# Kernel tuning notes

Hardware: AMD Instinct MI355X
Metric: run time of the kernel (lower is better)

Reference implementation:

```python
import jax, jax.numpy as jnp
import numpy as np

N, F, P, E, HID = 50000, 4, 12, 1_600_000, 64  # nodes, input feats, periods (FH), edges, hidden


def setup_inputs() -> dict:
    key = jax.random.key(0)
    ks = jax.random.split(key, 16)

    def nrm(k, shp, scale=0.1):
        return jax.random.normal(k, shp, jnp.float32) * scale

    inp = {
        "x": jax.random.normal(ks[0], (N, F, P), jnp.float32),
        "edge_index": jax.random.randint(ks[1], (2, E), 0, N),
        "edge_weights": jax.random.uniform(ks[2], (E,), jnp.float32),
        "att": nrm(ks[3], (P,), 1.0),
    }
    i = 4
    for g in ("z", "r", "h"):  # TGCN gate params: GCNConv weight/bias + Linear(2*hid, hid)
        inp[f"Wg_{g}"] = nrm(ks[i], (F, HID))
        inp[f"bg_{g}"] = jnp.zeros((HID,), jnp.float32)
        inp[f"Wl_{g}"] = nrm(jax.random.fold_in(ks[i], 1), (2 * HID, HID))
        inp[f"bl_{g}"] = jnp.zeros((HID,), jnp.float32)
        i += 1
    for j in range(1, 5):
        inp[f"W{j}"] = nrm(ks[i], (HID, HID))
        inp[f"b{j}"] = jnp.zeros((HID,), jnp.float32)
        i += 1
    inp["Wo"] = nrm(ks[i], (HID, P * F))
    inp["bo"] = jnp.zeros((P * F,), jnp.float32)
    return inp


def _gcn_norm(edge_index, ew):
    # GCNConv default: add self loops (weight 1), symmetric D^-1/2 (A+I) D^-1/2 normalization
    src, dst = edge_index[0], edge_index[1]
    loop = jnp.arange(N)
    src_f = jnp.concatenate([src, loop])
    dst_f = jnp.concatenate([dst, loop])
    ew_f = jnp.concatenate([ew, jnp.ones((N,), ew.dtype)])
    deg = jax.ops.segment_sum(ew_f, dst_f, num_segments=N)
    dinv = jnp.where(deg > 0, jax.lax.rsqrt(deg), 0.0)
    norm = dinv[src_f] * ew_f * dinv[dst_f]
    return src_f, dst_f, norm


def _gcn(x, W, b, src, dst, norm):
    xw = x @ W                               # [N, HID] transform before propagate
    msg = xw[src] * norm[:, None]            # gather + scale, [E+N, HID]
    return jax.ops.segment_sum(msg, dst, num_segments=N) + b


def reference(x, edge_index, edge_weights, att,
              Wg_z, bg_z, Wl_z, bl_z,
              Wg_r, bg_r, Wl_r, bl_r,
              Wg_h, bg_h, Wl_h, bl_h,
              W1, b1, W2, b2, W3, b3, W4, b4, Wo, bo):
    src, dst, norm = _gcn_norm(edge_index, edge_weights)

    def tgcn_cell(xt):
        # A3TGCN passes H=None every period -> H starts at zeros each period
        Hz = jnp.zeros((xt.shape[0], HID), xt.dtype)
        z = jax.nn.sigmoid(jnp.concatenate([_gcn(xt, Wg_z, bg_z, src, dst, norm), Hz], -1) @ Wl_z + bl_z)
        r = jax.nn.sigmoid(jnp.concatenate([_gcn(xt, Wg_r, bg_r, src, dst, norm), Hz], -1) @ Wl_r + bl_r)
        htil = jnp.tanh(jnp.concatenate([_gcn(xt, Wg_h, bg_h, src, dst, norm), Hz * r], -1) @ Wl_h + bl_h)
        return z * Hz + (1.0 - z) * htil

    probs = jax.nn.softmax(att)
    h = jnp.zeros((N, HID), x.dtype)
    for p in range(P):  # small fixed period loop keeps peak memory at one period's messages
        h = h + probs[p] * tgcn_cell(x[:, :, p])

    h = jax.nn.relu(h)
    h = h @ W1 + b1
    h = h @ W2 + b2
    h = h @ W3 + b3
    h = h @ W4 + b4
    h = h @ Wo + bo                          # [N, FH*F]
    return h.reshape(-1, F, P)
```

## Files before the change

### kernel.cpp

```cpp
#include <hip/hip_runtime.h>
#include <hip/hip_fp16.h>

#define FP 48
#define HID 64
#define NP 12
#define PL 65
#define NBLK 256
#define CAPB 9216

__device__ __forceinline__ void mm_stage(const float* __restrict__ Alds,
                                         const float* __restrict__ Wg,
                                         float* __restrict__ Clds, int t)
{
    const int rg = (t >> 4) * 4, cg = (t & 15) * 4;
    float acc[4][4] = {};
    for (int k = 0; k < 64; ++k) {
        float a0 = Alds[(rg + 0) * PL + k];
        float a1 = Alds[(rg + 1) * PL + k];
        float a2 = Alds[(rg + 2) * PL + k];
        float a3 = Alds[(rg + 3) * PL + k];
        const float4 bv = *reinterpret_cast<const float4*>(Wg + k * 64 + cg);
        acc[0][0] += a0 * bv.x; acc[0][1] += a0 * bv.y; acc[0][2] += a0 * bv.z; acc[0][3] += a0 * bv.w;
        acc[1][0] += a1 * bv.x; acc[1][1] += a1 * bv.y; acc[1][2] += a1 * bv.z; acc[1][3] += a1 * bv.w;
        acc[2][0] += a2 * bv.x; acc[2][1] += a2 * bv.y; acc[2][2] += a2 * bv.z; acc[2][3] += a2 * bv.w;
        acc[3][0] += a3 * bv.x; acc[3][1] += a3 * bv.y; acc[3][2] += a3 * bv.z; acc[3][3] += a3 * bv.w;
    }
    for (int i = 0; i < 4; ++i)
        for (int j = 0; j < 4; ++j)
            Clds[(rg + i) * PL + cg + j] = acc[i][j];
}

__device__ __forceinline__ void bias_stage(const float* __restrict__ bin,
                                           const float* __restrict__ Wg,
                                           const float* __restrict__ badd,
                                           float* __restrict__ bout, int t)
{
    if (t < 64) {
        float s = badd[t];
        for (int k = 0; k < 64; ++k) s += bin[k] * Wg[k * 64 + t];
        bout[t] = s;
    }
}

__device__ void do_prep(
    const float* __restrict__ att,
    const float* __restrict__ Wg_z, const float* __restrict__ bg_z,
    const float* __restrict__ Wl_z, const float* __restrict__ bl_z,
    const float* __restrict__ Wg_h, const float* __restrict__ bg_h,
    const float* __restrict__ Wl_h, const float* __restrict__ bl_h,
    const float* __restrict__ W1, const float* __restrict__ b1,
    const float* __restrict__ W2, const float* __restrict__ b2,
    const float* __restrict__ W3, const float* __restrict__ b3,
    const float* __restrict__ W4, const float* __restrict__ b4,
    const float* __restrict__ Wo, const float* __restrict__ bo,
    float* __restrict__ probs, float* __restrict__ Mz, float* __restrict__ cz,
    float* __restrict__ Mh, float* __restrict__ ch,
    float* __restrict__ Wc, float* __restrict__ bc, int t)
{
    __shared__ float A[64 * PL];
    __shared__ float B[64 * PL];
    __shared__ float bias[64];
    __shared__ float bias2[64];

    if (t == 0) {
        float m = att[0];
        for (int p = 1; p < NP; ++p) m = fmaxf(m, att[p]);
        float e[NP]; float s = 0.f;
        for (int p = 0; p < NP; ++p) { e[p] = __expf(att[p] - m); s += e[p]; }
        float inv = 1.f / s;
        for (int p = 0; p < NP; ++p) probs[p] = e[p] * inv;
    }

    {
        int f = t >> 6, j = t & 63;
        float az = 0.f, ah = 0.f;
        for (int k = 0; k < HID; ++k) {
            az += Wg_z[f * HID + k] * Wl_z[k * HID + j];
            ah += Wg_h[f * HID + k] * Wl_h[k * HID + j];
        }
        Mz[t] = az; Mh[t] = ah;
    }
    if (t < HID) {
        float az = bl_z[t], ah = bl_h[t];
        for (int k = 0; k < HID; ++k) {
            az += bg_z[k] * Wl_z[k * HID + t];
            ah += bg_h[k] * Wl_h[k * HID + t];
        }
        cz[t] = az; ch[t] = ah;
    }

    for (int idx = t; idx < 4096; idx += 256) {
        int i = idx >> 6, j = idx & 63;
        A[i * PL + j] = W1[idx];
    }
    if (t < 64) bias[t] = b1[t];
    __syncthreads();

    mm_stage(A, W2, B, t);
    bias_stage(bias, W2, b2, bias2, t);
    __syncthreads();
    mm_stage(B, W3, A, t);
    bias_stage(bias2, W3, b3, bias, t);
    __syncthreads();
    mm_stage(A, W4, B, t);
    bias_stage(bias, W4, b4, bias2, t);
    __syncthreads();

    const int rg = (t >> 4) * 4, cg = (t & 15) * 4;
    if (cg < FP) {
        float acc[4][4] = {};
        for (int k = 0; k < 64; ++k) {
            float a0 = B[(rg + 0) * PL + k];
            float a1 = B[(rg + 1) * PL + k];
            float a2 = B[(rg + 2) * PL + k];
            float a3 = B[(rg + 3) * PL + k];
            const float4 bv = *reinterpret_cast<const float4*>(Wo + k * FP + cg);
            acc[0][0] += a0 * bv.x; acc[0][1] += a0 * bv.y; acc[0][2] += a0 * bv.z; acc[0][3] += a0 * bv.w;
            acc[1][0] += a1 * bv.x; acc[1][1] += a1 * bv.y; acc[1][2] += a1 * bv.z; acc[1][3] += a1 * bv.w;
            acc[2][0] += a2 * bv.x; acc[2][1] += a2 * bv.y; acc[2][2] += a2 * bv.z; acc[2][3] += a2 * bv.w;
            acc[3][0] += a3 * bv.x; acc[3][1] += a3 * bv.y; acc[3][2] += a3 * bv.z; acc[3][3] += a3 * bv.w;
        }
        for (int i = 0; i < 4; ++i)
            for (int j = 0; j < 4; ++j)
                Wc[(rg + i) * FP + cg + j] = acc[i][j];
    }
    if (t < FP) {
        float s = bo[t];
        for (int k = 0; k < 64; ++k) s += bias2[k] * Wo[k * FP + t];
        bc[t] = s;
    }
}

__global__ __launch_bounds__(256) void build_kernel(
    const int* __restrict__ src, const int* __restrict__ dst,
    const float* __restrict__ ew,
    unsigned* __restrict__ cursor, int2* __restrict__ binned,
    int E, int CE, int NBUK,
    const float* __restrict__ att,
    const float* __restrict__ Wg_z, const float* __restrict__ bg_z,
    const float* __restrict__ Wl_z, const float* __restrict__ bl_z,
    const float* __restrict__ Wg_h, const float* __restrict__ bg_h,
    const float* __restrict__ Wl_h, const float* __restrict__ bl_h,
    const float* __restrict__ W1, const float* __restrict__ b1,
    const float* __restrict__ W2, const float* __restrict__ b2,
    const float* __restrict__ W3, const float* __restrict__ b3,
    const float* __restrict__ W4, const float* __restrict__ b4,
    const float* __restrict__ Wo, const float* __restrict__ bo,
    float* __restrict__ probs, float* __restrict__ Mz, float* __restrict__ cz,
    float* __restrict__ Mh, float* __restrict__ ch,
    float* __restrict__ Wc, float* __restrict__ bc)
{
    const int t = threadIdx.x;
    if (blockIdx.x == NBLK) {
        do_prep(att, Wg_z, bg_z, Wl_z, bl_z, Wg_h, bg_h, Wl_h, bl_h,
                W1, b1, W2, b2, W3, b3, W4, b4, Wo, bo,
                probs, Mz, cz, Mh, ch, Wc, bc, t);
        return;
    }
    __shared__ int cnt[256];
    __shared__ int off[256];
    for (int i = t; i < NBUK; i += 256) cnt[i] = 0;
    __syncthreads();
    const int base = blockIdx.x * CE;
    const int endb = min(base + CE, E);
    for (int e = base + t; e < endb; e += 256)
        atomicAdd(&cnt[((unsigned)dst[e]) >> 8], 1);
    __syncthreads();
    for (int i = t; i < NBUK; i += 256)
        off[i] = (int)atomicAdd(&cursor[i], (unsigned)cnt[i]);
    __syncthreads();
    for (int e = base + t; e < endb; e += 256) {
        const int d = dst[e];
        const int b = ((unsigned)d) >> 8;
        const int r = atomicAdd(&off[b], 1);
        if (r < CAPB)
            binned[(size_t)b * CAPB + r] =
                make_int2(((d & 255) << 16) | src[e], __float_as_int(ew[e]));
    }
}

__global__ __launch_bounds__(256) void csr_convert_kernel(
    const int2* __restrict__ binned, const unsigned* __restrict__ cursor,
    unsigned* __restrict__ csr, int2* __restrict__ nodeinfo,
    const float* __restrict__ x,
    unsigned short* __restrict__ xs, int N, int NBUK)
{
    const int t = threadIdx.x;
    const int b = blockIdx.x;
    const int node0 = b << 8;
    const int nend = min(256, N - node0);
    const int ebeg = b * CAPB;
    const int ecnt = min((int)cursor[b], CAPB);
    const int eend = ebeg + ecnt;

    __shared__ int   cnt[256];
    __shared__ float fsum[256];
    __shared__ int   pfx[256];
    __shared__ float sdi[256];

    cnt[t] = 0; fsum[t] = 0.f;
    __syncthreads();

    for (int e = ebeg + t; e < eend; e += 256) {
        const int2 v = binned[e];
        const int dl = (v.x >> 16) & 255;
        atomicAdd(&cnt[dl], 1);
        atomicAdd(&fsum[dl], __int_as_float(v.y));
    }
    __syncthreads();

    const int myc = cnt[t];
    pfx[t] = myc;
    __syncthreads();
    for (int off = 1; off < 256; off <<= 1) {
        int tmp = (t >= off) ? pfx[t - off] : 0;
        __syncthreads();
        pfx[t] += tmp;
        __syncthreads();
    }
    const int excl = pfx[t] - myc;

    const float di = rsqrtf(1.f + fsum[t]);
    sdi[t] = di;
    if (t < nend)
        nodeinfo[node0 + t] = make_int2((myc << 22) | (ebeg + excl), __float_as_int(di));

    cnt[t] = ebeg + excl;
    __syncthreads();

    for (int e = ebeg + t; e < eend; e += 256) {
        const int2 v = binned[e];
        const int dl = (v.x >> 16) & 255;
        const int pos = atomicAdd(&cnt[dl], 1);
        const float w = __int_as_float(v.y);
        const unsigned hb = (unsigned)__half_as_ushort(__float2half_rn(w));
        csr[pos] = (unsigned)(v.x & 0xffff) | (hb << 16);
    }

    const int gtot = nend * 6;
    for (int g = t; g < gtot; g += 256) {
        const int nl = g / 6;
        const int q = g - nl * 6;
        const float dsc = sdi[nl];
        const float* xr = x + (size_t)(node0 + nl) * FP + q * 8;
        const float4 v0 = *reinterpret_cast<const float4*>(xr);
        const float4 v1 = *reinterpret_cast<const float4*>(xr + 4);
        unsigned p0 = (unsigned)__half_as_ushort(__float2half_rn(dsc * v0.x)) |
                      ((unsigned)__half_as_ushort(__float2half_rn(dsc * v0.y)) << 16);
        unsigned p1 = (unsigned)__half_as_ushort(__float2half_rn(dsc * v0.z)) |
                      ((unsigned)__half_as_ushort(__float2half_rn(dsc * v0.w)) << 16);
        unsigned p2 = (unsigned)__half_as_ushort(__float2half_rn(dsc * v1.x)) |
                      ((unsigned)__half_as_ushort(__float2half_rn(dsc * v1.y)) << 16);
        unsigned p3 = (unsigned)__half_as_ushort(__float2half_rn(dsc * v1.z)) |
                      ((unsigned)__half_as_ushort(__float2half_rn(dsc * v1.w)) << 16);
        *reinterpret_cast<int4*>(xs + (size_t)(node0 + nl) * FP + q * 8) =
            make_int4((int)p0, (int)p1, (int)p2, (int)p3);
    }
}

__global__ __launch_bounds__(256) void gather_node_kernel(
    const unsigned short* __restrict__ xs, const float* __restrict__ x,
    const int2* __restrict__ nodeinfo,
    const unsigned* __restrict__ csr,
    const float* __restrict__ probs,
    const float* __restrict__ Mz, const float* __restrict__ cz,
    const float* __restrict__ Mh, const float* __restrict__ ch,
    const float* __restrict__ Wc, const float* __restrict__ bc,
    float* __restrict__ out, int N)
{
    __shared__ __align__(16) float sWc[HID * FP];
    __shared__ __align__(16) float sprobs[16];
    __shared__ __align__(16) float yacc[4][384];
    __shared__ __align__(16) float yld[4][FP];
    __shared__ __align__(16) float hld[4][HID];
    for (int i = threadIdx.x; i < HID * FP; i += 256) sWc[i] = Wc[i];
    if (threadIdx.x < NP) sprobs[threadIdx.x] = probs[threadIdx.x];
    __syncthreads();

    const int lane = threadIdx.x & 63;
    const int wib  = threadIdx.x >> 6;
    const int n    = blockIdx.x * 4 + wib;
    if (n >= N) return;

    const int slot = lane >> 3;
    const int q    = lane & 7;
    const bool act = (q < 6);
    const int qc   = act ? q : 5;
    const char* xsb = (const char*)xs;

    const int2 ni = nodeinfo[n];
    const int beg = ni.x & 0x3FFFFF;
    const int end = beg + ((unsigned)ni.x >> 22);
    const float di = __int_as_float(ni.y);

    float a0 = 0.f, a1 = 0.f, a2 = 0.f, a3 = 0.f;
    float a4 = 0.f, a5 = 0.f, a6 = 0.f, a7 = 0.f;
    #pragma unroll 2
    for (int e = beg + slot; e < end; e += 8) {
        const unsigned ev = csr[e];
        const float w = __half2float(__ushort_as_half((unsigned short)(ev >> 16)));
        const unsigned soff = (ev & 0xffffu) * 96u;
        const int4 xv = *reinterpret_cast<const int4*>(xsb + soff + (qc << 4));
        const float2 f0 = __half22float2(*reinterpret_cast<const __half2*>(&xv.x));
        const float2 f1 = __half22float2(*reinterpret_cast<const __half2*>(&xv.y));
        const float2 f2 = __half22float2(*reinterpret_cast<const __half2*>(&xv.z));
        const float2 f3 = __half22float2(*reinterpret_cast<const __half2*>(&xv.w));
        a0 = fmaf(w, f0.x, a0); a1 = fmaf(w, f0.y, a1);
        a2 = fmaf(w, f1.x, a2); a3 = fmaf(w, f1.y, a3);
        a4 = fmaf(w, f2.x, a4); a5 = fmaf(w, f2.y, a5);
        a6 = fmaf(w, f3.x, a6); a7 = fmaf(w, f3.y, a7);
    }

    if (act) {
        float* dst0 = &yacc[wib][slot * 48 + q * 8];
        *reinterpret_cast<float4*>(dst0)     = make_float4(a0, a1, a2, a3);
        *reinterpret_cast<float4*>(dst0 + 4) = make_float4(a4, a5, a6, a7);
    }

    if (lane < FP) {
        const float* yf = yacc[wib];
        float s = 0.f;
        #pragma unroll
        for (int sl = 0; sl < 8; ++sl) s += yf[sl * 48 + lane];
        float xself = x[(size_t)n * FP + lane];
        float yv = di * s + di * di * xself;
        int f = lane / 12;
        int p = lane - f * 12;
        yld[wib][p * 4 + f] = yv;
    }

    const float mz0 = Mz[lane], mz1 = Mz[64 + lane], mz2 = Mz[128 + lane], mz3 = Mz[192 + lane];
    const float mh0 = Mh[lane], mh1 = Mh[64 + lane], mh2 = Mh[128 + lane], mh3 = Mh[192 + lane];
    const float czv = cz[lane], chv = ch[lane];
    const int   c   = (lane < FP) ? lane : 0;
    const float bcv = bc[c];

    const float* yw = yld[wib];
    float hacc = 0.f;
    #pragma unroll
    for (int p = 0; p < NP; ++p) {
        const float4 v = *reinterpret_cast<const float4*>(yw + p * 4);
        float az = czv + v.x * mz0 + v.y * mz1 + v.z * mz2 + v.w * mz3;
        float ah = chv + v.x * mh0 + v.y * mh1 + v.z * mh2 + v.w * mh3;
        float g  = __builtin_amdgcn_rcpf(1.f + __expf(az));
        float ahc = fminf(fmaxf(ah, -15.f), 15.f);
        float eh = __expf(2.f * ahc);
        float th = 1.f - 2.f * __builtin_amdgcn_rcpf(eh + 1.f);
        hacc += sprobs[p] * g * th;
    }
    hacc = fmaxf(hacc, 0.f);

    hld[wib][lane] = hacc;
    const float* hw = hld[wib];
    float o = bcv;
    #pragma unroll
    for (int i4 = 0; i4 < 16; ++i4) {
        const float4 h4 = *reinterpret_cast<const float4*>(hw + i4 * 4);
        o += h4.x * sWc[(i4 * 4 + 0) * FP + c];
        o += h4.y * sWc[(i4 * 4 + 1) * FP + c];
        o += h4.z * sWc[(i4 * 4 + 2) * FP + c];
        o += h4.w * sWc[(i4 * 4 + 3) * FP + c];
    }
    if (lane < FP) out[(size_t)n * FP + lane] = o;
}

extern "C" void kernel_launch(void* const* d_in, const int* in_sizes, int n_in,
                              void* d_out, int out_size, void* d_ws, size_t ws_size,
                              hipStream_t stream)
{
    const int N = in_sizes[0] / FP;
    const int E = in_sizes[1] / 2;
    const int NBUK = (N + 255) >> 8;
    const int CE = (E + NBLK - 1) / NBLK;

    const float* x    = (const float*)d_in[0];
    const int*   ei   = (const int*)d_in[1];
    const float* ew   = (const float*)d_in[2];
    const float* att  = (const float*)d_in[3];
    const float* Wg_z = (const float*)d_in[4];
    const float* bg_z = (const float*)d_in[5];
    const float* Wl_z = (const float*)d_in[6];
    const float* bl_z = (const float*)d_in[7];
    const float* Wg_h = (const float*)d_in[12];
    const float* bg_h = (const float*)d_in[13];
    const float* Wl_h = (const float*)d_in[14];
    const float* bl_h = (const float*)d_in[15];
    const float* W1 = (const float*)d_in[16]; const float* b1 = (const float*)d_in[17];
    const float* W2 = (const float*)d_in[18]; const float* b2 = (const float*)d_in[19];
    const float* W3 = (const float*)d_in[20]; const float* b3 = (const float*)d_in[21];
    const float* W4 = (const float*)d_in[22]; const float* b4 = (const float*)d_in[23];
    const float* Wo = (const float*)d_in[24]; const float* bo = (const float*)d_in[25];

    const int* srcp = ei;
    const int* dstp = ei + E;

    int2* binned       = (int2*)d_ws;
    unsigned* csr      = (unsigned*)(binned + (size_t)NBUK * CAPB);
    unsigned short* xs = (unsigned short*)(csr + (size_t)NBUK * CAPB);
    unsigned* cursor   = (unsigned*)(xs + (size_t)N * FP);
    int2* nodeinfo     = (int2*)(cursor + 256);
    float* probs       = (float*)(nodeinfo + N);
    float* Mz          = probs + 16;
    float* cz          = Mz + 256;
    float* Mh          = cz + 64;
    float* ch          = Mh + 256;
    float* Wc          = ch + 64;
    float* bc          = Wc + HID * FP;

    hipMemsetAsync(cursor, 0, (size_t)NBUK * sizeof(unsigned), stream);

    build_kernel<<<NBLK + 1, 256, 0, stream>>>(
        srcp, dstp, ew, cursor, binned, E, CE, NBUK,
        att, Wg_z, bg_z, Wl_z, bl_z, Wg_h, bg_h, Wl_h, bl_h,
        W1, b1, W2, b2, W3, b3, W4, b4, Wo, bo,
        probs, Mz, cz, Mh, ch, Wc, bc);

    csr_convert_kernel<<<NBUK, 256, 0, stream>>>(binned, cursor, csr, nodeinfo,
                                                 x, xs, N, NBUK);

    gather_node_kernel<<<(N + 3) / 4, 256, 0, stream>>>(xs, x, nodeinfo, csr,
                                                        probs, Mz, cz, Mh, ch, Wc, bc,
                                                        (float*)d_out, N);
}
```

Before: 252.2 us.

## Fuse build, CSR convert and gather into one cooperative persistent kernel

Replaces the memset and three kernel launches with a single cooperative kernel that uses grid-wide syncs between phases: binning, per-quarter histogramming, CSR scatter plus x prescaling, and the node gather/MLP. The CSR convert phase is split into four work items per bucket, with partial counts exchanged through global memory, to expose more parallelism than one block per bucket. The binning phase uses up to 768 blocks instead of 256. The aim is to cut launch gaps and raise parallelism in the conversion step, at the cost of grid.sync overhead, a persistent-loop gather that is capped by occupancy, and one block doing the weight prep serially.

```diff
diff --git a/kernel.cpp b/kernel.cpp
--- a/kernel.cpp
+++ b/kernel.cpp
@@ -1,25 +1,41 @@
 #include <hip/hip_runtime.h>
 #include <hip/hip_fp16.h>
+#include <hip/hip_cooperative_groups.h>
+
+namespace cg = cooperative_groups;
 
 #define FP 48
 #define HID 64
 #define NP 12
 #define PL 65
-#define NBLK 256
 #define CAPB 9216
-
-__device__ __forceinline__ void mm_stage(const float* __restrict__ Alds,
-                                         const float* __restrict__ Wg,
-                                         float* __restrict__ Clds, int t)
+#define NBUILD 768
+
+struct Params {
+    const float* x; const int* src; const int* dst; const float* ew;
+    const float* att;
+    const float *Wg_z, *bg_z, *Wl_z, *bl_z;
+    const float *Wg_h, *bg_h, *Wl_h, *bl_h;
+    const float *W1, *b1, *W2, *b2, *W3, *b3, *W4, *b4, *Wo, *bo;
+    float *probs, *Mz, *cz, *Mh, *ch, *Wc, *bc, *G;
+    unsigned* cursor; int2* binned; unsigned* csr; int2* nodeinfo;
+    int* qcnt; float* qfsum;
+    unsigned short* xs; float* out;
+    int N, E, NBUK, NQ;
+};
+
+__device__ __forceinline__ void mm_stage_g(const float* __restrict__ Alds,
+                                           const float* __restrict__ Wg,
+                                           float* __restrict__ Cg, int t)
 {
-    const int rg = (t >> 4) * 4, cg = (t & 15) * 4;
+    const int rg = (t >> 4) * 4, cgx = (t & 15) * 4;
     float acc[4][4] = {};
     for (int k = 0; k < 64; ++k) {
         float a0 = Alds[(rg + 0) * PL + k];
         float a1 = Alds[(rg + 1) * PL + k];
         float a2 = Alds[(rg + 2) * PL + k];
         float a3 = Alds[(rg + 3) * PL + k];
-        const float4 bv = *reinterpret_cast<const float4*>(Wg + k * 64 + cg);
+        const float4 bv = *reinterpret_cast<const float4*>(Wg + k * 64 + cgx);
         acc[0][0] += a0 * bv.x; acc[0][1] += a0 * bv.y; acc[0][2] += a0 * bv.z; acc[0][3] += a0 * bv.w;
         acc[1][0] += a1 * bv.x; acc[1][1] += a1 * bv.y; acc[1][2] += a1 * bv.z; acc[1][3] += a1 * bv.w;
         acc[2][0] += a2 * bv.x; acc[2][1] += a2 * bv.y; acc[2][2] += a2 * bv.z; acc[2][3] += a2 * bv.w;
@@ -27,7 +43,7 @@
     }
     for (int i = 0; i < 4; ++i)
         for (int j = 0; j < 4; ++j)
-            Clds[(rg + i) * PL + cg + j] = acc[i][j];
+            Cg[(rg + i) * 64 + cgx + j] = acc[i][j];
 }
 
 __device__ __forceinline__ void bias_stage(const float* __restrict__ bin,
@@ -42,79 +58,65 @@
     }
 }
 
-__device__ void do_prep(
-    const float* __restrict__ att,
-    const float* __restrict__ Wg_z, const float* __restrict__ bg_z,
-    const float* __restrict__ Wl_z, const float* __restrict__ bl_z,
-    const float* __restrict__ Wg_h, const float* __restrict__ bg_h,
-    const float* __restrict__ Wl_h, const float* __restrict__ bl_h,
-    const float* __restrict__ W1, const float* __restrict__ b1,
-    const float* __restrict__ W2, const float* __restrict__ b2,
-    const float* __restrict__ W3, const float* __restrict__ b3,
-    const float* __restrict__ W4, const float* __restrict__ b4,
-    const float* __restrict__ Wo, const float* __restrict__ bo,
-    float* __restrict__ probs, float* __restrict__ Mz, float* __restrict__ cz,
-    float* __restrict__ Mh, float* __restrict__ ch,
-    float* __restrict__ Wc, float* __restrict__ bc, int t)
+__device__ void do_prep(const Params& p, float* smem, int t)
 {
-    __shared__ float A[64 * PL];
-    __shared__ float B[64 * PL];
-    __shared__ float bias[64];
-    __shared__ float bias2[64];
+    float* A = smem;
+    float* bias = smem + 64 * PL;
+    float* bias2 = bias + 64;
 
     if (t == 0) {
-        float m = att[0];
-        for (int p = 1; p < NP; ++p) m = fmaxf(m, att[p]);
+        float m = p.att[0];
+        for (int q = 1; q < NP; ++q) m = fmaxf(m, p.att[q]);
         float e[NP]; float s = 0.f;
-        for (int p = 0; p < NP; ++p) { e[p] = __expf(att[p] - m); s += e[p]; }
+        for (int q = 0; q < NP; ++q) { e[q] = __expf(p.att[q] - m); s += e[q]; }
         float inv = 1.f / s;
-        for (int p = 0; p < NP; ++p) probs[p] = e[p] * inv;
-    }
-
+        for (int q = 0; q < NP; ++q) p.probs[q] = e[q] * inv;
+    }
     {
         int f = t >> 6, j = t & 63;
         float az = 0.f, ah = 0.f;
         for (int k = 0; k < HID; ++k) {
-            az += Wg_z[f * HID + k] * Wl_z[k * HID + j];
-            ah += Wg_h[f * HID + k] * Wl_h[k * HID + j];
-        }
-        Mz[t] = az; Mh[t] = ah;
+            az += p.Wg_z[f * HID + k] * p.Wl_z[k * HID + j];
+            ah += p.Wg_h[f * HID + k] * p.Wl_h[k * HID + j];
+        }
+        p.Mz[t] = az; p.Mh[t] = ah;
     }
     if (t < HID) {
-        float az = bl_z[t], ah = bl_h[t];
+        float az = p.bl_z[t], ah = p.bl_h[t];
         for (int k = 0; k < HID; ++k) {
-            az += bg_z[k] * Wl_z[k * HID + t];
-            ah += bg_h[k] * Wl_h[k * HID + t];
-        }
-        cz[t] = az; ch[t] = ah;
-    }
-
-    for (int idx = t; idx < 4096; idx += 256) {
-        int i = idx >> 6, j = idx & 63;
-        A[i * PL + j] = W1[idx];
-    }
-    if (t < 64) bias[t] = b1[t];
-    __syncthreads();
-
-    mm_stage(A, W2, B, t);
-    bias_stage(bias, W2, b2, bias2, t);
-    __syncthreads();
-    mm_stage(B, W3, A, t);
-    bias_stage(bias2, W3, b3, bias, t);
-    __syncthreads();
-    mm_stage(A, W4, B, t);
-    bias_stage(bias, W4, b4, bias2, t);
-    __syncthreads();
-
-    const int rg = (t >> 4) * 4, cg = (t & 15) * 4;
-    if (cg < FP) {
+            az += p.bg_z[k] * p.Wl_z[k * HID + t];
+            ah += p.bg_h[k] * p.Wl_h[k * HID + t];
+        }
+        p.cz[t] = az; p.ch[t] = ah;
+    }
+
+    for (int idx = t; idx < 4096; idx += 256)
+        A[(idx >> 6) * PL + (idx & 63)] = p.W1[idx];
+    if (t < 64) bias[t] = p.b1[t];
+    __syncthreads();
+
+    mm_stage_g(A, p.W2, p.G, t);  bias_stage(bias, p.W2, p.b2, bias2, t);
+    __syncthreads();
+    for (int idx = t; idx < 4096; idx += 256) A[(idx >> 6) * PL + (idx & 63)] = p.G[idx];
+    __syncthreads();
+    mm_stage_g(A, p.W3, p.G, t);  bias_stage(bias2, p.W3, p.b3, bias, t);
+    __syncthreads();
+    for (int idx = t; idx < 4096; idx += 256) A[(idx >> 6) * PL + (idx & 63)] = p.G[idx];
+    __syncthreads();
+    mm_stage_g(A, p.W4, p.G, t);  bias_stage(bias, p.W4, p.b4, bias2, t);
+    __syncthreads();
+    for (int idx = t; idx < 4096; idx += 256) A[(idx >> 6) * PL + (idx & 63)] = p.G[idx];
+    __syncthreads();
+
+    const int rg = (t >> 4) * 4, cgx = (t & 15) * 4;
+    if (cgx < FP) {
         float acc[4][4] = {};
         for (int k = 0; k < 64; ++k) {
-            float a0 = B[(rg + 0) * PL + k];
-            float a1 = B[(rg + 1) * PL + k];
-            float a2 = B[(rg + 2) * PL + k];
-            float a3 = B[(rg + 3) * PL + k];
-            const float4 bv = *reinterpret_cast<const float4*>(Wo + k * FP + cg);
+            float a0 = A[(rg + 0) * PL + k];
+            float a1 = A[(rg + 1) * PL + k];
+            float a2 = A[(rg + 2) * PL + k];
+            float a3 = A[(rg + 3) * PL + k];
+            const float4 bv = *reinterpret_cast<const float4*>(p.Wo + k * FP + cgx);
             acc[0][0] += a0 * bv.x; acc[0][1] += a0 * bv.y; acc[0][2] += a0 * bv.z; acc[0][3] += a0 * bv.w;
             acc[1][0] += a1 * bv.x; acc[1][1] += a1 * bv.y; acc[1][2] += a1 * bv.z; acc[1][3] += a1 * bv.w;
             acc[2][0] += a2 * bv.x; acc[2][1] += a2 * bv.y; acc[2][2] += a2 * bv.z; acc[2][3] += a2 * bv.w;
@@ -122,246 +124,255 @@
         }
         for (int i = 0; i < 4; ++i)
             for (int j = 0; j < 4; ++j)
-                Wc[(rg + i) * FP + cg + j] = acc[i][j];
+                p.Wc[(rg + i) * FP + cgx + j] = acc[i][j];
     }
     if (t < FP) {
-        float s = bo[t];
-        for (int k = 0; k < 64; ++k) s += bias2[k] * Wo[k * FP + t];
-        bc[t] = s;
+        float s = p.bo[t];
+        for (int k = 0; k < 64; ++k) s += bias2[k] * p.Wo[k * FP + t];
+        p.bc[t] = s;
     }
 }
 
-__global__ __launch_bounds__(256) void build_kernel(
-    const int* __restrict__ src, const int* __restrict__ dst,
-    const float* __restrict__ ew,
-    unsigned* __restrict__ cursor, int2* __restrict__ binned,
-    int E, int CE, int NBUK,
-    const float* __restrict__ att,
-    const float* __restrict__ Wg_z, const float* __restrict__ bg_z,
-    const float* __restrict__ Wl_z, const float* __restrict__ bl_z,
-    const float* __restrict__ Wg_h, const float* __restrict__ bg_h,
-    const float* __restrict__ Wl_h, const float* __restrict__ bl_h,
-    const float* __restrict__ W1, const float* __restrict__ b1,
-    const float* __restrict__ W2, const float* __restrict__ b2,
-    const float* __restrict__ W3, const float* __restrict__ b3,
-    const float* __restrict__ W4, const float* __restrict__ b4,
-    const float* __restrict__ Wo, const float* __restrict__ bo,
-    float* __restrict__ probs, float* __restrict__ Mz, float* __restrict__ cz,
-    float* __restrict__ Mh, float* __restrict__ ch,
-    float* __restrict__ Wc, float* __restrict__ bc)
+__global__ __launch_bounds__(256, 4) void fused_all(Params p)
 {
+    cg::grid_group grid = cg::this_grid();
+    __shared__ __align__(16) float smem[5072];
     const int t = threadIdx.x;
-    if (blockIdx.x == NBLK) {
-        do_prep(att, Wg_z, bg_z, Wl_z, bl_z, Wg_h, bg_h, Wl_h, bl_h,
-                W1, b1, W2, b2, W3, b3, W4, b4, Wo, bo,
-                probs, Mz, cz, Mh, ch, Wc, bc, t);
-        return;
-    }
-    __shared__ int cnt[256];
-    __shared__ int off[256];
-    for (int i = t; i < NBUK; i += 256) cnt[i] = 0;
-    __syncthreads();
-    const int base = blockIdx.x * CE;
-    const int endb = min(base + CE, E);
-    for (int e = base + t; e < endb; e += 256)
-        atomicAdd(&cnt[((unsigned)dst[e]) >> 8], 1);
-    __syncthreads();
-    for (int i = t; i < NBUK; i += 256)
-        off[i] = (int)atomicAdd(&cursor[i], (unsigned)cnt[i]);
-    __syncthreads();
-    for (int e = base + t; e < endb; e += 256) {
-        const int d = dst[e];
-        const int b = ((unsigned)d) >> 8;
-        const int r = atomicAdd(&off[b], 1);
-        if (r < CAPB)
-            binned[(size_t)b * CAPB + r] =
-                make_int2(((d & 255) << 16) | src[e], __float_as_int(ew[e]));
-    }
-}
-
-__global__ __launch_bounds__(256) void csr_convert_kernel(
-    const int2* __restrict__ binned, const unsigned* __restrict__ cursor,
-    unsigned* __restrict__ csr, int2* __restrict__ nodeinfo,
-    const float* __restrict__ x,
-    unsigned short* __restrict__ xs, int N, int NBUK)
-{
-    const int t = threadIdx.x;
-    const int b = blockIdx.x;
-    const int node0 = b << 8;
-    const int nend = min(256, N - node0);
-    const int ebeg = b * CAPB;
-    const int ecnt = min((int)cursor[b], CAPB);
-    const int eend = ebeg + ecnt;
-
-    __shared__ int   cnt[256];
-    __shared__ float fsum[256];
-    __shared__ int   pfx[256];
-    __shared__ float sdi[256];
-
-    cnt[t] = 0; fsum[t] = 0.f;
-    __syncthreads();
-
-    for (int e = ebeg + t; e < eend; e += 256) {
-        const int2 v = binned[e];
-        const int dl = (v.x >> 16) & 255;
-        atomicAdd(&cnt[dl], 1);
-        atomicAdd(&fsum[dl], __int_as_float(v.y));
-    }
-    __syncthreads();
-
-    const int myc = cnt[t];
-    pfx[t] = myc;
-    __syncthreads();
-    for (int off = 1; off < 256; off <<= 1) {
-        int tmp = (t >= off) ? pfx[t - off] : 0;
+    const int bid = blockIdx.x;
+
+    if (bid == 0) p.cursor[t] = 0u;
+    grid.sync();
+
+    if (bid == 0) {
+        do_prep(p, smem, t);
+    } else {
+        const int nbuild = min((int)gridDim.x - 1, NBUILD);
+        const int rb = bid - 1;
+        if (rb < nbuild) {
+            int* bcnt = (int*)smem;
+            int* boff = (int*)smem + 256;
+            const int ce = (p.E + nbuild - 1) / nbuild;
+            const int base = rb * ce;
+            const int endb = min(base + ce, p.E);
+            bcnt[t] = 0;
+            __syncthreads();
+            for (int e = base + t; e < endb; e += 256)
+                atomicAdd(&bcnt[((unsigned)p.dst[e]) >> 8], 1);
+            __syncthreads();
+            if (t < p.NBUK) {
+                const int c = bcnt[t];
+                boff[t] = c ? (int)atomicAdd(&p.cursor[t], (unsigned)c) : 0;
+            }
+            __syncthreads();
+            for (int e = base + t; e < endb; e += 256) {
+                const int d = p.dst[e];
+                const int b = ((unsigned)d) >> 8;
+                const int r = atomicAdd(&boff[b], 1);
+                if (r < CAPB)
+                    p.binned[(size_t)b * CAPB + r] =
+                        make_int2(((d & 255) << 16) | p.src[e], __float_as_int(p.ew[e]));
+            }
+        }
+    }
+    grid.sync();
+
+    {
+        int* cnt = (int*)smem;
+        float* fsum = smem + 256;
+        const int NW = p.NBUK * 4;
+        for (int w = bid; w < NW; w += gridDim.x) {
+            const int b = w >> 2, s = w & 3;
+            const int ebeg = b * CAPB;
+            const int ecnt = min((int)p.cursor[b], CAPB);
+            const int q0 = (ecnt * s) >> 2, q1 = (ecnt * (s + 1)) >> 2;
+            cnt[t] = 0; fsum[t] = 0.f;
+            __syncthreads();
+            for (int e = ebeg + q0 + t; e < ebeg + q1; e += 256) {
+                const int2 v = p.binned[e];
+                const int dl = (v.x >> 16) & 255;
+                atomicAdd(&cnt[dl], 1);
+                atomicAdd(&fsum[dl], __int_as_float(v.y));
+            }
+            __syncthreads();
+            p.qcnt[w * 256 + t] = cnt[t];
+            p.qfsum[w * 256 + t] = fsum[t];
+            __syncthreads();
+        }
+    }
+    grid.sync();
+
+    {
+        int* cnt = (int*)smem;
+        int* pfx = (int*)smem + 256;
+        float* sdi = smem + 512;
+        const int NW = p.NBUK * 4;
+        for (int w = bid; w < NW; w += gridDim.x) {
+            const int b = w >> 2, s = w & 3;
+            const int node0 = b << 8;
+            const int nend = min(256, p.N - node0);
+            const int ebeg = b * CAPB;
+            const int ecnt = min((int)p.cursor[b], CAPB);
+            const int q0 = (ecnt * s) >> 2, q1 = (ecnt * (s + 1)) >> 2;
+
+            const int c0 = p.qcnt[(b * 4 + 0) * 256 + t];
+            const int c1 = p.qcnt[(b * 4 + 1) * 256 + t];
+            const int c2 = p.qcnt[(b * 4 + 2) * 256 + t];
+            const int c3 = p.qcnt[(b * 4 + 3) * 256 + t];
+            const float fs = (p.qfsum[(b * 4 + 0) * 256 + t] + p.qfsum[(b * 4 + 1) * 256 + t])
+                           + (p.qfsum[(b * 4 + 2) * 256 + t] + p.qfsum[(b * 4 + 3) * 256 + t]);
+            const int myc = c0 + c1 + c2 + c3;
+            pfx[t] = myc;
+            __syncthreads();
+            for (int off = 1; off < 256; off <<= 1) {
+                int tmp = (t >= off) ? pfx[t - off] : 0;
+                __syncthreads();
+                pfx[t] += tmp;
+                __syncthreads();
+            }
+            const int start = ebeg + pfx[t] - myc;
+            const float di = rsqrtf(1.f + fs);
+            sdi[t] = di;
+            int mybase = start;
+            if (s > 0) mybase += c0;
+            if (s > 1) mybase += c1;
+            if (s > 2) mybase += c2;
+            cnt[t] = mybase;
+            if (s == 0 && t < nend)
+                p.nodeinfo[node0 + t] = make_int2((myc << 22) | start, __float_as_int(di));
+            __syncthreads();
+
+            for (int e = ebeg + q0 + t; e < ebeg + q1; e += 256) {
+                const int2 v = p.binned[e];
+                const int dl = (v.x >> 16) & 255;
+                const int pos = atomicAdd(&cnt[dl], 1);
+                const float wv = __int_as_float(v.y);
+                const unsigned hb = (unsigned)__half_as_ushort(__float2half_rn(wv));
+                p.csr[pos] = (unsigned)(v.x & 0xffff) | (hb << 16);
+            }
+
+            const int nlo = s * 64;
+            const int nhi = min(nlo + 64, nend);
+            const int gtot = (nhi - nlo) * 6;
+            for (int g = t; g < gtot; g += 256) {
+                const int gl = g / 6;
+                const int nl = nlo + gl;
+                const int qq = g - gl * 6;
+                const float dsc = sdi[nl];
+                const float* xr = p.x + (size_t)(node0 + nl) * FP + qq * 8;
+                const float4 v0 = *reinterpret_cast<const float4*>(xr);
+                const float4 v1 = *reinterpret_cast<const float4*>(xr + 4);
+                unsigned w0 = (unsigned)__half_as_ushort(__float2half_rn(dsc * v0.x)) |
+                              ((unsigned)__half_as_ushort(__float2half_rn(dsc * v0.y)) << 16);
+                unsigned w1 = (unsigned)__half_as_ushort(__float2half_rn(dsc * v0.z)) |
+                              ((unsigned)__half_as_ushort(__float2half_rn(dsc * v0.w)) << 16);
+                unsigned w2 = (unsigned)__half_as_ushort(__float2half_rn(dsc * v1.x)) |
+                              ((unsigned)__half_as_ushort(__float2half_rn(dsc * v1.y)) << 16);
+                unsigned w3 = (unsigned)__half_as_ushort(__float2half_rn(dsc * v1.z)) |
+                              ((unsigned)__half_as_ushort(__float2half_rn(dsc * v1.w)) << 16);
+                *reinterpret_cast<int4*>(p.xs + (size_t)(node0 + nl) * FP + qq * 8) =
+                    make_int4((int)w0, (int)w1, (int)w2, (int)w3);
+            }
+            __syncthreads();
+        }
+    }
+    grid.sync();
+
+    {
+        float* sWc = smem;
+        float* sprobs = smem + 3072;
+        const int lane = t & 63;
+        const int wib = t >> 6;
+        float* yaccw = smem + 3088 + wib * 384;
+        float* yldw  = smem + 4624 + wib * 48;
+        float* hldw  = smem + 4816 + wib * 64;
+
+        for (int i = t; i < HID * FP; i += 256) sWc[i] = p.Wc[i];
+        if (t < NP) sprobs[t] = p.probs[t];
         __syncthreads();
-        pfx[t] += tmp;
-        __syncthreads();
-    }
-    const int excl = pfx[t] - myc;
-
-    const float di = rsqrtf(1.f + fsum[t]);
-    sdi[t] = di;
-    if (t < nend)
-        nodeinfo[node0 + t] = make_int2((myc << 22) | (ebeg + excl), __float_as_int(di));
-
-    cnt[t] = ebeg + excl;
-    __syncthreads();
-
-    for (int e = ebeg + t; e < eend; e += 256) {
-        const int2 v = binned[e];
-        const int dl = (v.x >> 16) & 255;
-        const int pos = atomicAdd(&cnt[dl], 1);
-        const float w = __int_as_float(v.y);
-        const unsigned hb = (unsigned)__half_as_ushort(__float2half_rn(w));
-        csr[pos] = (unsigned)(v.x & 0xffff) | (hb << 16);
-    }
-
-    const int gtot = nend * 6;
-    for (int g = t; g < gtot; g += 256) {
-        const int nl = g / 6;
-        const int q = g - nl * 6;
-        const float dsc = sdi[nl];
-        const float* xr = x + (size_t)(node0 + nl) * FP + q * 8;
-        const float4 v0 = *reinterpret_cast<const float4*>(xr);
-        const float4 v1 = *reinterpret_cast<const float4*>(xr + 4);
-        unsigned p0 = (unsigned)__half_as_ushort(__float2half_rn(dsc * v0.x)) |
-                      ((unsigned)__half_as_ushort(__float2half_rn(dsc * v0.y)) << 16);
-        unsigned p1 = (unsigned)__half_as_ushort(__float2half_rn(dsc * v0.z)) |
-                      ((unsigned)__half_as_ushort(__float2half_rn(dsc * v0.w)) << 16);
-        unsigned p2 = (unsigned)__half_as_ushort(__float2half_rn(dsc * v1.x)) |
-                      ((unsigned)__half_as_ushort(__float2half_rn(dsc * v1.y)) << 16);
-        unsigned p3 = (unsigned)__half_as_ushort(__float2half_rn(dsc * v1.z)) |
-                      ((unsigned)__half_as_ushort(__float2half_rn(dsc * v1.w)) << 16);
-        *reinterpret_cast<int4*>(xs + (size_t)(node0 + nl) * FP + q * 8) =
-            make_int4((int)p0, (int)p1, (int)p2, (int)p3);
-    }
-}
-
-__global__ __launch_bounds__(256) void gather_node_kernel(
-    const unsigned short* __restrict__ xs, const float* __restrict__ x,
-    const int2* __restrict__ nodeinfo,
-    const unsigned* __restrict__ csr,
-    const float* __restrict__ probs,
-    const float* __restrict__ Mz, const float* __restrict__ cz,
-    const float* __restrict__ Mh, const float* __restrict__ ch,
-    const float* __restrict__ Wc, const float* __restrict__ bc,
-    float* __restrict__ out, int N)
-{
-    __shared__ __align__(16) float sWc[HID * FP];
-    __shared__ __align__(16) float sprobs[16];
-    __shared__ __align__(16) float yacc[4][384];
-    __shared__ __align__(16) float yld[4][FP];
-    __shared__ __align__(16) float hld[4][HID];
-    for (int i = threadIdx.x; i < HID * FP; i += 256) sWc[i] = Wc[i];
-    if (threadIdx.x < NP) sprobs[threadIdx.x] = probs[threadIdx.x];
-    __syncthreads();
-
-    const int lane = threadIdx.x & 63;
-    const int wib  = threadIdx.x >> 6;
-    const int n    = blockIdx.x * 4 + wib;
-    if (n >= N) return;
-
-    const int slot = lane >> 3;
-    const int q    = lane & 7;
-    const bool act = (q < 6);
-    const int qc   = act ? q : 5;
-    const char* xsb = (const char*)xs;
-
-    const int2 ni = nodeinfo[n];
-    const int beg = ni.x & 0x3FFFFF;
-    const int end = beg + ((unsigned)ni.x >> 22);
-    const float di = __int_as_float(ni.y);
-
-    float a0 = 0.f, a1 = 0.f, a2 = 0.f, a3 = 0.f;
-    float a4 = 0.f, a5 = 0.f, a6 = 0.f, a7 = 0.f;
-    #pragma unroll 2
-    for (int e = beg + slot; e < end; e += 8) {
-        const unsigned ev = csr[e];
-        const float w = __half2float(__ushort_as_half((unsigned short)(ev >> 16)));
-        const unsigned soff = (ev & 0xffffu) * 96u;
-        const int4 xv = *reinterpret_cast<const int4*>(xsb + soff + (qc << 4));
-        const float2 f0 = __half22float2(*reinterpret_cast<const __half2*>(&xv.x));
-        const float2 f1 = __half22float2(*reinterpret_cast<const __half2*>(&xv.y));
-        const float2 f2 = __half22float2(*reinterpret_cast<const __half2*>(&xv.z));
-        const float2 f3 = __half22float2(*reinterpret_cast<const __half2*>(&xv.w));
-        a0 = fmaf(w, f0.x, a0); a1 = fmaf(w, f0.y, a1);
-        a2 = fmaf(w, f1.x, a2); a3 = fmaf(w, f1.y, a3);
-        a4 = fmaf(w, f2.x, a4); a5 = fmaf(w, f2.y, a5);
-        a6 = fmaf(w, f3.x, a6); a7 = fmaf(w, f3.y, a7);
-    }
-
-    if (act) {
-        float* dst0 = &yacc[wib][slot * 48 + q * 8];
-        *reinterpret_cast<float4*>(dst0)     = make_float4(a0, a1, a2, a3);
-        *reinterpret_cast<float4*>(dst0 + 4) = make_float4(a4, a5, a6, a7);
-    }
-
-    if (lane < FP) {
-        const float* yf = yacc[wib];
-        float s = 0.f;
-        #pragma unroll
-        for (int sl = 0; sl < 8; ++sl) s += yf[sl * 48 + lane];
-        float xself = x[(size_t)n * FP + lane];
-        float yv = di * s + di * di * xself;
-        int f = lane / 12;
-        int p = lane - f * 12;
-        yld[wib][p * 4 + f] = yv;
-    }
-
-    const float mz0 = Mz[lane], mz1 = Mz[64 + lane], mz2 = Mz[128 + lane], mz3 = Mz[192 + lane];
-    const float mh0 = Mh[lane], mh1 = Mh[64 + lane], mh2 = Mh[128 + lane], mh3 = Mh[192 + lane];
-    const float czv = cz[lane], chv = ch[lane];
-    const int   c   = (lane < FP) ? lane : 0;
-    const float bcv = bc[c];
-
-    const float* yw = yld[wib];
-    float hacc = 0.f;
-    #pragma unroll
-    for (int p = 0; p < NP; ++p) {
-        const float4 v = *reinterpret_cast<const float4*>(yw + p * 4);
-        float az = czv + v.x * mz0 + v.y * mz1 + v.z * mz2 + v.w * mz3;
-        float ah = chv + v.x * mh0 + v.y * mh1 + v.z * mh2 + v.w * mh3;
-        float g  = __builtin_amdgcn_rcpf(1.f + __expf(az));
-        float ahc = fminf(fmaxf(ah, -15.f), 15.f);
-        float eh = __expf(2.f * ahc);
-        float th = 1.f - 2.f * __builtin_amdgcn_rcpf(eh + 1.f);
-        hacc += sprobs[p] * g * th;
-    }
-    hacc = fmaxf(hacc, 0.f);
-
-    hld[wib][lane] = hacc;
-    const float* hw = hld[wib];
-    float o = bcv;
-    #pragma unroll
-    for (int i4 = 0; i4 < 16; ++i4) {
-        const float4 h4 = *reinterpret_cast<const float4*>(hw + i4 * 4);
-        o += h4.x * sWc[(i4 * 4 + 0) * FP + c];
-        o += h4.y * sWc[(i4 * 4 + 1) * FP + c];
-        o += h4.z * sWc[(i4 * 4 + 2) * FP + c];
-        o += h4.w * sWc[(i4 * 4 + 3) * FP + c];
-    }
-    if (lane < FP) out[(size_t)n * FP + lane] = o;
+
+        const int slot = lane >> 3;
+        const int q = lane & 7;
+        const bool act = (q < 6);
+        const int qc = act ? q : 5;
+        const char* xsb = (const char*)p.xs;
+
+        const float mz0 = p.Mz[lane], mz1 = p.Mz[64 + lane], mz2 = p.Mz[128 + lane], mz3 = p.Mz[192 + lane];
+        const float mh0 = p.Mh[lane], mh1 = p.Mh[64 + lane], mh2 = p.Mh[128 + lane], mh3 = p.Mh[192 + lane];
+        const float czv = p.cz[lane], chv = p.ch[lane];
+        const int c = (lane < FP) ? lane : 0;
+        const float bcv = p.bc[c];
+
+        for (int g = bid; g < p.NQ; g += gridDim.x) {
+            const int n = g * 4 + wib;
+            if (n >= p.N) continue;
+
+            const int2 ni = p.nodeinfo[n];
+            const int beg = ni.x & 0x3FFFFF;
+            const int end = beg + (int)((unsigned)ni.x >> 22);
+            const float di = __int_as_float(ni.y);
+
+            float a0 = 0.f, a1 = 0.f, a2 = 0.f, a3 = 0.f;
+            float a4 = 0.f, a5 = 0.f, a6 = 0.f, a7 = 0.f;
+            #pragma unroll 2
+            for (int e = beg + slot; e < end; e += 8) {
+                const unsigned ev = p.csr[e];
+                const float w = __half2float(__ushort_as_half((unsigned short)(ev >> 16)));
+                const unsigned soff = (ev & 0xffffu) * 96u;
+                const int4 xv = *reinterpret_cast<const int4*>(xsb + soff + (qc << 4));
+                const float2 f0 = __half22float2(*reinterpret_cast<const __half2*>(&xv.x));
+                const float2 f1 = __half22float2(*reinterpret_cast<const __half2*>(&xv.y));
+                const float2 f2 = __half22float2(*reinterpret_cast<const __half2*>(&xv.z));
+                const float2 f3 = __half22float2(*reinterpret_cast<const __half2*>(&xv.w));
+                a0 = fmaf(w, f0.x, a0); a1 = fmaf(w, f0.y, a1);
+                a2 = fmaf(w, f1.x, a2); a3 = fmaf(w, f1.y, a3);
+                a4 = fmaf(w, f2.x, a4); a5 = fmaf(w, f2.y, a5);
+                a6 = fmaf(w, f3.x, a6); a7 = fmaf(w, f3.y, a7);
+            }
+
+            if (act) {
+                float* dst0 = &yaccw[slot * 48 + q * 8];
+                *reinterpret_cast<float4*>(dst0)     = make_float4(a0, a1, a2, a3);
+                *reinterpret_cast<float4*>(dst0 + 4) = make_float4(a4, a5, a6, a7);
+            }
+
+            if (lane < FP) {
+                float s = 0.f;
+                #pragma unroll
+                for (int sl = 0; sl < 8; ++sl) s += yaccw[sl * 48 + lane];
+                float xself = p.x[(size_t)n * FP + lane];
+                float yv = di * s + di * di * xself;
+                int f = lane / 12;
+                int pp = lane - f * 12;
+                yldw[pp * 4 + f] = yv;
+            }
+
+            float hacc = 0.f;
+            #pragma unroll
+            for (int pp = 0; pp < NP; ++pp) {
+                const float4 v = *reinterpret_cast<const float4*>(yldw + pp * 4);
+                float az = czv + v.x * mz0 + v.y * mz1 + v.z * mz2 + v.w * mz3;
+                float ah = chv + v.x * mh0 + v.y * mh1 + v.z * mh2 + v.w * mh3;
+                float gg = __builtin_amdgcn_rcpf(1.f + __expf(az));
+                float ahc = fminf(fmaxf(ah, -15.f), 15.f);
+                float eh = __expf(2.f * ahc);
+                float th = 1.f - 2.f * __builtin_amdgcn_rcpf(eh + 1.f);
+                hacc += sprobs[pp] * gg * th;
+            }
+            hacc = fmaxf(hacc, 0.f);
+
+            hldw[lane] = hacc;
+            float o = bcv;
+            #pragma unroll
+            for (int i4 = 0; i4 < 16; ++i4) {
+                const float4 h4 = *reinterpret_cast<const float4*>(hldw + i4 * 4);
+                o += h4.x * sWc[(i4 * 4 + 0) * FP + c];
+                o += h4.y * sWc[(i4 * 4 + 1) * FP + c];
+                o += h4.z * sWc[(i4 * 4 + 2) * FP + c];
+                o += h4.w * sWc[(i4 * 4 + 3) * FP + c];
+            }
+            if (lane < FP) p.out[(size_t)n * FP + lane] = o;
+        }
+    }
 }
 
 extern "C" void kernel_launch(void* const* d_in, const int* in_sizes, int n_in,
@@ -371,35 +382,18 @@
     const int N = in_sizes[0] / FP;
     const int E = in_sizes[1] / 2;
     const int NBUK = (N + 255) >> 8;
-    const int CE = (E + NBLK - 1) / NBLK;
-
-    const float* x    = (const float*)d_in[0];
-    const int*   ei   = (const int*)d_in[1];
-    const float* ew   = (const float*)d_in[2];
-    const float* att  = (const float*)d_in[3];
-    const float* Wg_z = (const float*)d_in[4];
-    const float* bg_z = (const float*)d_in[5];
-    const float* Wl_z = (const float*)d_in[6];
-    const float* bl_z = (const float*)d_in[7];
-    const float* Wg_h = (const float*)d_in[12];
-    const float* bg_h = (const float*)d_in[13];
-    const float* Wl_h = (const float*)d_in[14];
-    const float* bl_h = (const float*)d_in[15];
-    const float* W1 = (const float*)d_in[16]; const float* b1 = (const float*)d_in[17];
-    const float* W2 = (const float*)d_in[18]; const float* b2 = (const float*)d_in[19];
-    const float* W3 = (const float*)d_in[20]; const float* b3 = (const float*)d_in[21];
-    const float* W4 = (const float*)d_in[22]; const float* b4 = (const float*)d_in[23];
-    const float* Wo = (const float*)d_in[24]; const float* bo = (const float*)d_in[25];
-
-    const int* srcp = ei;
-    const int* dstp = ei + E;
+
+    const int* ei = (const int*)d_in[1];
 
     int2* binned       = (int2*)d_ws;
     unsigned* csr      = (unsigned*)(binned + (size_t)NBUK * CAPB);
     unsigned short* xs = (unsigned short*)(csr + (size_t)NBUK * CAPB);
     unsigned* cursor   = (unsigned*)(xs + (size_t)N * FP);
     int2* nodeinfo     = (int2*)(cursor + 256);
-    float* probs       = (float*)(nodeinfo + N);
+    int* qcnt          = (int*)(nodeinfo + N);
+    float* qfsum       = (float*)(qcnt + NBUK * 4 * 256);
+    float* G           = qfsum + NBUK * 4 * 256;
+    float* probs       = G + 4096;
     float* Mz          = probs + 16;
     float* cz          = Mz + 256;
     float* Mh          = cz + 64;
@@ -407,18 +401,44 @@
     float* Wc          = ch + 64;
     float* bc          = Wc + HID * FP;
 
-    hipMemsetAsync(cursor, 0, (size_t)NBUK * sizeof(unsigned), stream);
-
-    build_kernel<<<NBLK + 1, 256, 0, stream>>>(
-        srcp, dstp, ew, cursor, binned, E, CE, NBUK,
-        att, Wg_z, bg_z, Wl_z, bl_z, Wg_h, bg_h, Wl_h, bl_h,
-        W1, b1, W2, b2, W3, b3, W4, b4, Wo, bo,
-        probs, Mz, cz, Mh, ch, Wc, bc);
-
-    csr_convert_kernel<<<NBUK, 256, 0, stream>>>(binned, cursor, csr, nodeinfo,
-                                                 x, xs, N, NBUK);
-
-    gather_node_kernel<<<(N + 3) / 4, 256, 0, stream>>>(xs, x, nodeinfo, csr,
-                                                        probs, Mz, cz, Mh, ch, Wc, bc,
-                                                        (float*)d_out, N);
+    Params hp;
+    hp.x = (const float*)d_in[0];
+    hp.src = ei; hp.dst = ei + E;
+    hp.ew = (const float*)d_in[2];
+    hp.att = (const float*)d_in[3];
+    hp.Wg_z = (const float*)d_in[4];  hp.bg_z = (const float*)d_in[5];
+    hp.Wl_z = (const float*)d_in[6];  hp.bl_z = (const float*)d_in[7];
+    hp.Wg_h = (const float*)d_in[12]; hp.bg_h = (const float*)d_in[13];
+    hp.Wl_h = (const float*)d_in[14]; hp.bl_h = (const float*)d_in[15];
+    hp.W1 = (const float*)d_in[16]; hp.b1 = (const float*)d_in[17];
+    hp.W2 = (const float*)d_in[18]; hp.b2 = (const float*)d_in[19];
+    hp.W3 = (const float*)d_in[20]; hp.b3 = (const float*)d_in[21];
+    hp.W4 = (const float*)d_in[22]; hp.b4 = (const float*)d_in[23];
+    hp.Wo = (const float*)d_in[24]; hp.bo = (const float*)d_in[25];
+    hp.probs = probs; hp.Mz = Mz; hp.cz = cz; hp.Mh = Mh; hp.ch = ch;
+    hp.Wc = Wc; hp.bc = bc; hp.G = G;
+    hp.cursor = cursor; hp.binned = binned; hp.csr = csr; hp.nodeinfo = nodeinfo;
+    hp.qcnt = qcnt; hp.qfsum = qfsum;
+    hp.xs = xs; hp.out = (float*)d_out;
+    hp.N = N; hp.E = E; hp.NBUK = NBUK; hp.NQ = (N + 3) / 4;
+
+    static int gridBlocks = 0;
+    if (gridBlocks == 0) {
+        int bpc = 0;
+        if (hipOccupancyMaxActiveBlocksPerMultiprocessor(&bpc, (const void*)fused_all,
+                                                         256, 0) != hipSuccess || bpc < 1)
+            bpc = 4;
+        int ncu = 256;
+        hipDeviceProp_t prop;
+        int dev = 0;
+        if (hipGetDevice(&dev) == hipSuccess &&
+            hipGetDeviceProperties(&prop, dev) == hipSuccess &&
+            prop.multiProcessorCount > 0)
+            ncu = prop.multiProcessorCount;
+        gridBlocks = bpc * ncu;
+    }
+
+    void* args[] = { (void*)&hp };
+    hipLaunchCooperativeKernel((const void*)fused_all, dim3(gridBlocks), dim3(256),
+                               args, 0, stream);
 }
```

After: 557.2 us. +120.9%, slower.
